# Kernel tuning notes

Measured on AMD Instinct MI355X. Metric: run time of the kernel, lower is better.

## Reference

```python
import jax, jax.numpy as jnp
import numpy as np

B, S1, S2, D1, D2 = 4, 2048, 2048, 512, 512
H, DK, DV = 8, 64, 64


def setup_inputs() -> dict:
    key = jax.random.key(0)
    ks = jax.random.split(key, 8)
    x1 = jax.random.normal(ks[0], (B, S1, D1), dtype=jnp.float32)
    x2 = jax.random.normal(ks[1], (B, S2, D2), dtype=jnp.float32)
    x3 = jax.random.normal(ks[2], (B, S2, D2), dtype=jnp.float32)
    s = 0.02
    Wq = jax.random.normal(ks[3], (D1, H * DK), dtype=jnp.float32) * s
    Wk = jax.random.normal(ks[4], (D2, H * DK), dtype=jnp.float32) * s
    Wv = jax.random.normal(ks[5], (D2, H * DV), dtype=jnp.float32) * s
    Wo = jax.random.normal(ks[6], (H * DV, D1), dtype=jnp.float32) * s
    bo = jnp.zeros((D1,), dtype=jnp.float32)
    return {"x1": x1, "x2": x2, "x3": x3, "Wq": Wq, "Wk": Wk, "Wv": Wv, "Wo": Wo, "bo": bo}


def reference(x1, x2, x3, Wq, Wk, Wv, Wo, bo):
    b, s1, _ = x1.shape
    # project to per-head q, k, v: [B, H, S, Dh]
    q = (x1 @ Wq).reshape(b, s1, H, DK).transpose(0, 2, 1, 3)
    k = (x2 @ Wk).reshape(b, x2.shape[1], H, DK).transpose(0, 2, 1, 3)
    v = (x3 @ Wv).reshape(b, x3.shape[1], H, DV).transpose(0, 2, 1, 3)
    scores = jnp.einsum('bhqd,bhkd->bhqk', q, k) / jnp.sqrt(jnp.float32(DK))
    attn = jax.nn.softmax(scores, axis=-1)
    out = jnp.einsum('bhqk,bhkd->bhqd', attn, v)  # [B, H, S1, DV]
    out = out.transpose(0, 2, 1, 3).reshape(b, s1, H * DV)
    return out @ Wo + bo
```

## Files before the change

kernel.cpp:

```cpp
#include <hip/hip_runtime.h>

typedef __attribute__((ext_vector_type(4))) float f32x4;
typedef __attribute__((ext_vector_type(16))) float f32x16;
typedef __attribute__((ext_vector_type(8))) __bf16 bf16x8;
typedef __attribute__((ext_vector_type(4))) __bf16 bf16x4;
typedef __attribute__((ext_vector_type(2))) __bf16 bf16x2;
typedef __attribute__((ext_vector_type(4))) unsigned u32x4;

#define DEVINL __device__ __forceinline__

DEVINL void gld16(const void* g, void* l) {
  __builtin_amdgcn_global_load_lds((__attribute__((address_space(1))) void*)(void*)g,
                                   (__attribute__((address_space(3))) void*)l, 16, 0, 0);
}


__global__ __launch_bounds__(256) void cvt_w(const float* Wq, const float* Wk, const float* Wv,
                                             const float* Wo, __bf16* WT) {
  __shared__ float t[64][65];
  const int l = blockIdx.x;
  const int z = l >> 6;
  const float* W = z == 0 ? Wq : z == 1 ? Wk : z == 2 ? Wv : Wo;
  __bf16* D = WT + (size_t)z * 512 * 512;
  const int r0 = ((l >> 3) & 7) * 64, c0 = (l & 7) * 64;
  const int tx = threadIdx.x & 63, ty = threadIdx.x >> 6;
#pragma unroll
  for (int j = 0; j < 16; ++j)
    t[ty + j * 4][tx] = W[(size_t)(r0 + ty + j * 4) * 512 + c0 + tx];
  __syncthreads();
#pragma unroll
  for (int j = 0; j < 16; ++j)
    D[(size_t)(c0 + ty + j * 4) * 512 + r0 + tx] = (__bf16)t[tx][ty + j * 4];
}


DEVINL void gemm_tile_f32(const float* A, const __bf16* Bt, int m0, int n0,
                          __bf16* As, __bf16* Bs, f32x4 acc[4][4]) {
  const int tid = threadIdx.x, lane = tid & 63, w = tid >> 6;
  const int qd = lane >> 4, r = lane & 15;
  const int wm = w & 1, wn = w >> 1;
  const char* bp[4];
#pragma unroll
  for (int j = 0; j < 4; ++j) {
    int c = (w * 4 + j) * 64 + lane;
    int row = c >> 3, gc = (c & 7) ^ (row & 7);
    bp[j] = (const char*)Bt + (size_t)(n0 + row) * 1024 + gc * 16;
  }
  const int am = tid >> 4, ac = tid & 15;
  const float* ap = A + (size_t)(m0 + am) * 512 + ac * 4;
  int woff[8];
#pragma unroll
  for (int j = 0; j < 8; ++j) {
    int m = j * 16 + am;
    woff[j] = m * 128 + (((ac >> 1) ^ (m & 7)) << 4) + ((ac & 1) << 3);
  }
  int offA[4][2], offB[4][2];
#pragma unroll
  for (int t = 0; t < 4; ++t)
#pragma unroll
    for (int ks = 0; ks < 2; ++ks) {
      int m = wm * 64 + t * 16 + r;
      offA[t][ks] = m * 128 + (((ks * 4 + qd) ^ (m & 7)) * 16);
      int n = wn * 64 + t * 16 + r;
      offB[t][ks] = n * 128 + (((ks * 4 + qd) ^ (n & 7)) * 16);
    }
  char* AsC = (char*)As;
  char* BsC = (char*)Bs;
  f32x4 areg[8];
  auto loadA = [&](int kt) {
#pragma unroll
    for (int j = 0; j < 8; ++j)
      areg[j] = *(const f32x4*)(ap + (size_t)j * 16 * 512 + kt * 64);
  };
  loadA(0);
  for (int kt = 0; kt < 8; ++kt) {
    __syncthreads();
#pragma unroll
    for (int j = 0; j < 4; ++j) gld16(bp[j] + kt * 128, BsC + (w * 4 + j) * 1024);
#pragma unroll
    for (int j = 0; j < 8; ++j) {
      bf16x4 o;
#pragma unroll
      for (int g = 0; g < 4; ++g) o[g] = (__bf16)areg[j][g];
      *(bf16x4*)(AsC + woff[j]) = o;
    }
    if (kt < 7) loadA(kt + 1);
    __syncthreads();
#pragma unroll
    for (int ks = 0; ks < 2; ++ks) {
      bf16x8 a[4], b[4];
#pragma unroll
      for (int t = 0; t < 4; ++t) {
        a[t] = *(const bf16x8*)(AsC + offA[t][ks]);
        b[t] = *(const bf16x8*)(BsC + offB[t][ks]);
      }
#pragma unroll
      for (int i = 0; i < 4; ++i)
#pragma unroll
        for (int j2 = 0; j2 < 4; ++j2)
          acc[i][j2] = __builtin_amdgcn_mfma_f32_16x16x32_bf16(a[i], b[j2], acc[i][j2], 0, 0, 0);
    }
  }
}

__global__ __launch_bounds__(256, 3) void gemm_proj(const float* x1, const float* x2,
                                                    const float* x3, const __bf16* WT,
                                                    __bf16* Qo, __bf16* Ko, __bf16* Vto) {
  __shared__ __align__(16) char smem[34816];
  __bf16* As = (__bf16*)smem;
  __bf16* Bs = (__bf16*)(smem + 16384);
  const int z = blockIdx.z;
  const float* A = z == 0 ? x1 : z == 1 ? x2 : x3;
  const __bf16* Bt = WT + (size_t)z * 512 * 512;
  const int l = blockIdx.x;
  const int sidx = l >> 3;
  const int m0 = ((l & 7) * 8 + (sidx >> 2)) * 128;
  const int n0 = (sidx & 3) * 128;
  f32x4 acc[4][4] = {};
  gemm_tile_f32(A, Bt, m0, n0, As, Bs, acc);
  const int tid = threadIdx.x, lane = tid & 63, w = tid >> 6;
  const int qd = lane >> 4, r = lane & 15, wm = w & 1, wn = w >> 1;
  const int b = m0 >> 11, sbase = m0 & 2047;
  if (z == 2) {
    __syncthreads();
    char* T = smem;
#pragma unroll
    for (int mt = 0; mt < 4; ++mt)
#pragma unroll
      for (int nt = 0; nt < 4; ++nt) {
        int dv = wn * 64 + nt * 16 + r;
        int sl = wm * 64 + mt * 16 + qd * 4;
        bf16x4 p4;
#pragma unroll
        for (int g = 0; g < 4; ++g) p4[g] = (__bf16)acc[mt][nt][g];
        *(bf16x4*)(T + (size_t)dv * 272 + sl * 2) = p4;
      }
    __syncthreads();
#pragma unroll
    for (int p2 = 0; p2 < 2; ++p2) {
      int dvrow = p2 * 64 + (tid >> 2);
      int col = n0 + dvrow, h = col >> 6, d = col & 63;
      __bf16* dst = Vto + ((size_t)(b * 8 + h) * 64 + d) * 2048 + sbase + (tid & 3) * 8;
#pragma unroll
      for (int j = 0; j < 4; ++j) {
        bf16x8 vv = *(const bf16x8*)(T + (size_t)dvrow * 272 + (tid & 3) * 16 + j * 64);
        *(bf16x8*)(dst + j * 32) = vv;
      }
    }
  } else {
    const float qscale = 0.18033688f;
#pragma unroll
    for (int mt = 0; mt < 4; ++mt) {
#pragma unroll
      for (int nt = 0; nt < 4; ++nt) {
        f32x4 v = acc[mt][nt];
        if (z == 0) {
#pragma unroll
          for (int g = 0; g < 4; ++g) v[g] *= qscale;
        }
        int col = n0 + wn * 64 + nt * 16 + r;
        int h = col >> 6, d = col & 63;
        int s = sbase + wm * 64 + mt * 16 + qd * 4;
        __bf16* O = (z == 0 ? Qo : Ko) + ((size_t)(b * 8 + h) * 2048 + s) * 64 + d;
#pragma unroll
        for (int g = 0; g < 4; ++g) O[(size_t)g * 64] = (__bf16)v[g];
      }
    }
  }
}

__global__ __launch_bounds__(256, 2) void gemm_out(const __bf16* Op, const float* Lp,
                                                   const __bf16* WoT, const float* bo,
                                                   float* out) {
  __shared__ __align__(16) __bf16 As[64 * 64];
  __shared__ __align__(16) __bf16 Bs[128 * 64];
  const int tid = threadIdx.x, lane = tid & 63, w = tid >> 6;
  const int qd = lane >> 4, r = lane & 15, wm = w & 1, wn = w >> 1;
  const int id = blockIdx.x;
  const int rest = id >> 3;
  const int m0 = ((id & 7) * 16 + (rest & 15)) * 64;
  const int n0 = (rest >> 4) * 128;
  const int b8 = (m0 >> 11) * 8;
  const int sb = m0 & 2047;
  const char* bp[4];
#pragma unroll
  for (int j = 0; j < 4; ++j) {
    int c = (w * 4 + j) * 64 + lane;
    int row = c >> 3, gc = (c & 7) ^ (row & 7);
    bp[j] = (const char*)WoT + (size_t)(n0 + row) * 1024 + gc * 16;
  }
  int arow[2], ach[2];
#pragma unroll
  for (int j = 0; j < 2; ++j) {
    int c = (w * 2 + j) * 64 + lane;
    arow[j] = c >> 3;
    ach[j] = c & 7;
  }
  int offA[2][2], offB[4][2];
#pragma unroll
  for (int ks = 0; ks < 2; ++ks) {
#pragma unroll
    for (int t = 0; t < 2; ++t) {
      int m = wm * 32 + t * 16 + r;
      offA[t][ks] = m * 128 + (((ks * 4 + qd) ^ (m & 7)) * 16);
    }
#pragma unroll
    for (int t = 0; t < 4; ++t) {
      int n = wn * 64 + t * 16 + r;
      offB[t][ks] = n * 128 + (((ks * 4 + qd) ^ (n & 7)) * 16);
    }
  }
  char* AsC = (char*)As;
  char* BsC = (char*)Bs;
  bf16x8 pa0[2], pa1[2];
  float pinv[2];
  auto loadA = [&](int h) {
#pragma unroll
    for (int j = 0; j < 2; ++j) {
      size_t rr = (size_t)(b8 + h) * 2048 + sb + arow[j];
      const __bf16* p0 = Op + rr * 64 + ach[j] * 8;
      pa0[j] = *(const bf16x8*)p0;
      pa1[j] = *(const bf16x8*)(p0 + (size_t)32 * 2048 * 64);
      pinv[j] = 1.0f / (Lp[rr] + Lp[rr + 65536]);
    }
  };
  loadA(0);
  f32x4 acc[2][4] = {};
  for (int kt = 0; kt < 8; ++kt) {
    __syncthreads();
#pragma unroll
    for (int j = 0; j < 4; ++j) gld16(bp[j] + kt * 128, BsC + (w * 4 + j) * 1024);
#pragma unroll
    for (int j = 0; j < 2; ++j) {
      bf16x8 q;
#pragma unroll
      for (int k2 = 0; k2 < 8; ++k2)
        q[k2] = (__bf16)(((float)pa0[j][k2] + (float)pa1[j][k2]) * pinv[j]);
      *(bf16x8*)(AsC + arow[j] * 128 + (ach[j] ^ (arow[j] & 7)) * 16) = q;
    }
    __syncthreads();
    if (kt < 7) loadA(kt + 1);
#pragma unroll
    for (int ks = 0; ks < 2; ++ks) {
      bf16x8 a[2], b[4];
#pragma unroll
      for (int t = 0; t < 2; ++t) a[t] = *(const bf16x8*)(AsC + offA[t][ks]);
#pragma unroll
      for (int t = 0; t < 4; ++t) b[t] = *(const bf16x8*)(BsC + offB[t][ks]);
#pragma unroll
      for (int i = 0; i < 2; ++i)
#pragma unroll
        for (int j2 = 0; j2 < 4; ++j2)
          acc[i][j2] = __builtin_amdgcn_mfma_f32_16x16x32_bf16(a[i], b[j2], acc[i][j2], 0, 0, 0);
    }
  }
#pragma unroll
  for (int nt = 0; nt < 4; ++nt) {
    int col = n0 + wn * 64 + nt * 16 + r;
    float bv = bo[col];
#pragma unroll
    for (int mt = 0; mt < 2; ++mt) {
      int mg = m0 + wm * 32 + mt * 16 + qd * 4;
#pragma unroll
      for (int g = 0; g < 4; ++g) out[(size_t)(mg + g) * 512 + col] = acc[mt][nt][g] + bv;
    }
  }
}

__global__ __launch_bounds__(256, 4) void attn(const __bf16* Q, const __bf16* K,
                                               const __bf16* Vt, __bf16* Opart, float* Lp) {
  __shared__ __align__(16) __bf16 Qs[128 * 64];
  __shared__ __align__(16) __bf16 Ksd[2][64 * 64];
  __shared__ __align__(16) __bf16 Vs[64 * 64];
  const int tid = threadIdx.x, lane = tid & 63, w = tid >> 6;
  const int l31 = lane & 31, lh = lane >> 5;
  const int id = blockIdx.x;
  const int rest = id >> 3;
  const int bh = (id & 7) * 4 + (rest >> 5);
  const int kvh = (rest >> 4) & 1;
  const int q0 = (rest & 15) * 128;
  const char* QgC = (const char*)(Q + ((size_t)bh * 2048 + q0) * 64);
  const char* KgC = (const char*)(K + (size_t)bh * 2048 * 64);
  const char* VgC = (const char*)(Vt + (size_t)bh * 64 * 2048);
  char* QsC = (char*)Qs;
  char* VsC = (char*)Vs;
  char* Kc = (char*)Ksd;
  char* Kn = (char*)Ksd + 8192;

  int koff[2], voff[2], ldso[2];
#pragma unroll
  for (int j = 0; j < 2; ++j) {
    int c = (w * 2 + j) * 64 + lane;
    int m = c >> 3, gc = (c & 7) ^ (m & 7);
    int ms = (m & ~12) | ((m & 4) << 1) | ((m & 8) >> 1);
    koff[j] = ms * 128 + gc * 16;
    voff[j] = m * 4096 + gc * 16;
    ldso[j] = (w * 2 + j) * 1024;
  }

  const int kt0 = kvh * 16;
  const size_t kb = (size_t)kt0 * 8192;
  const size_t vb = (size_t)kt0 * 128;

#pragma unroll
  for (int j = 0; j < 4; ++j) {
    int c = (w * 4 + j) * 64 + lane;
    int m = c >> 3, gc = (c & 7) ^ (m & 7);
    gld16(QgC + m * 128 + gc * 16, QsC + (w * 4 + j) * 1024);
  }
  gld16(KgC + kb + koff[0], Kc + ldso[0]);
  gld16(KgC + kb + koff[1], Kc + ldso[1]);
  gld16(VgC + vb + voff[0], VsC + ldso[0]);
  gld16(VgC + vb + voff[1], VsC + ldso[1]);
  gld16(KgC + kb + 8192 + koff[0], Kn + ldso[0]);
  gld16(KgC + kb + 8192 + koff[1], Kn + ldso[1]);
  __builtin_amdgcn_sched_barrier(0);
  asm volatile("s_waitcnt vmcnt(2)" ::: "memory");
  __builtin_amdgcn_sched_barrier(0);
  __builtin_amdgcn_s_barrier();
  __builtin_amdgcn_sched_barrier(0);

  const int rb = l31 * 128;
  const int he = (((lane & 7) ^ lh) << 4);
  const int qrow = (w * 32 + l31) * 128;

  bf16x8 ones;
#pragma unroll
  for (int j = 0; j < 8; ++j) ones[j] = (__bf16)1.0f;

  f32x16 oacc[2] = {};
  f32x16 lacc = {};
  bf16x8 pa[4];

  auto smhalf = [&](const f32x16& s, bf16x8& pa0, bf16x8& pa1) {
    unsigned wds[8];
#pragma unroll
    for (int i = 0; i < 8; ++i) {
      bf16x2 t;
      t[0] = (__bf16)__builtin_exp2f(s[2 * i]);
      t[1] = (__bf16)__builtin_exp2f(s[2 * i + 1]);
      wds[i] = __builtin_bit_cast(unsigned, t);
    }
    pa0 = __builtin_bit_cast(bf16x8, (u32x4){wds[0], wds[1], wds[2], wds[3]});
    pa1 = __builtin_bit_cast(bf16x8, (u32x4){wds[4], wds[5], wds[6], wds[7]});
  };
  auto qkchain = [&](const char* Kb, int half, const bf16x8 qf[4]) {
    f32x16 s = {};
#pragma unroll
    for (int c = 0; c < 4; ++c) {
      bf16x8 kf = *(const bf16x8*)(Kb + half * 4096 + rb + ((c << 5) ^ he));
      s = __builtin_amdgcn_mfma_f32_32x32x16_bf16(kf, qf[c], s, 0, 0, 0);
    }
    return s;
  };

  {
    bf16x8 qf[4];
#pragma unroll
    for (int c = 0; c < 4; ++c) qf[c] = *(const bf16x8*)(QsC + qrow + ((c << 5) ^ he));
    f32x16 s0 = qkchain(Kc, 0, qf);
    f32x16 s1 = qkchain(Kc, 1, qf);
    smhalf(s0, pa[0], pa[1]);
    smhalf(s1, pa[2], pa[3]);
  }
  __builtin_amdgcn_sched_barrier(0);
  asm volatile("s_waitcnt vmcnt(0)" ::: "memory");
  __builtin_amdgcn_sched_barrier(0);
  __builtin_amdgcn_s_barrier();
  __builtin_amdgcn_sched_barrier(0);

#pragma unroll 1
  for (int t = 0; t < 15; ++t) {
    __builtin_amdgcn_s_setprio(1);
#pragma unroll
    for (int c = 0; c < 4; ++c) {
      lacc = __builtin_amdgcn_mfma_f32_32x32x16_bf16(pa[c], ones, lacc, 0, 0, 0);
      bf16x8 vf0 = *(const bf16x8*)(VsC + rb + ((c << 5) ^ he));
      oacc[0] = __builtin_amdgcn_mfma_f32_32x32x16_bf16(pa[c], vf0, oacc[0], 0, 0, 0);
      bf16x8 vf1 = *(const bf16x8*)(VsC + 4096 + rb + ((c << 5) ^ he));
      oacc[1] = __builtin_amdgcn_mfma_f32_32x32x16_bf16(pa[c], vf1, oacc[1], 0, 0, 0);
    }
    bf16x8 qf[4];
#pragma unroll
    for (int c = 0; c < 4; ++c) qf[c] = *(const bf16x8*)(QsC + qrow + ((c << 5) ^ he));
    f32x16 s0 = qkchain(Kn, 0, qf);
    f32x16 s1 = qkchain(Kn, 1, qf);
    smhalf(s0, pa[0], pa[1]);
    __builtin_amdgcn_s_setprio(0);
    __builtin_amdgcn_sched_barrier(0);
    __builtin_amdgcn_s_barrier();
    __builtin_amdgcn_sched_barrier(0);

    gld16(VgC + vb + (size_t)(t + 1) * 128 + voff[0], VsC + ldso[0]);
    gld16(VgC + vb + (size_t)(t + 1) * 128 + voff[1], VsC + ldso[1]);
    if (t < 14) {
      gld16(KgC + kb + (size_t)(t + 2) * 8192 + koff[0], Kc + ldso[0]);
      gld16(KgC + kb + (size_t)(t + 2) * 8192 + koff[1], Kc + ldso[1]);
    }
    __builtin_amdgcn_sched_barrier(0);
    smhalf(s1, pa[2], pa[3]);
    __builtin_amdgcn_sched_barrier(0);
    asm volatile("s_waitcnt vmcnt(0)" ::: "memory");
    __builtin_amdgcn_sched_barrier(0);
    __builtin_amdgcn_s_barrier();
    __builtin_amdgcn_sched_barrier(0);

    char* tmp = Kc;
    Kc = Kn;
    Kn = tmp;
  }

#pragma unroll
  for (int c = 0; c < 4; ++c) {
    lacc = __builtin_amdgcn_mfma_f32_32x32x16_bf16(pa[c], ones, lacc, 0, 0, 0);
    bf16x8 vf0 = *(const bf16x8*)(VsC + rb + ((c << 5) ^ he));
    oacc[0] = __builtin_amdgcn_mfma_f32_32x32x16_bf16(pa[c], vf0, oacc[0], 0, 0, 0);
    bf16x8 vf1 = *(const bf16x8*)(VsC + 4096 + rb + ((c << 5) ^ he));
    oacc[1] = __builtin_amdgcn_mfma_f32_32x32x16_bf16(pa[c], vf1, oacc[1], 0, 0, 0);
  }

  const size_t pbase = (size_t)(kvh * 32 + bh) * 2048;
  if (l31 == 0) {
#pragma unroll
    for (int g = 0; g < 16; ++g)
      Lp[pbase + q0 + w * 32 + (g & 3) + 8 * (g >> 2) + 4 * lh] = lacc[g];
  }
  __bf16* Ob0 = Opart + pbase * 64;
#pragma unroll
  for (int dvt = 0; dvt < 2; ++dvt) {
#pragma unroll
    for (int g = 0; g < 16; ++g) {
      int s = q0 + w * 32 + (g & 3) + 8 * (g >> 2) + 4 * lh;
      Ob0[(size_t)s * 64 + dvt * 32 + l31] = (__bf16)oacc[dvt][g];
    }
  }
}


extern "C" void kernel_launch(void* const* d_in, const int* in_sizes, int n_in,
                              void* d_out, int out_size, void* d_ws, size_t ws_size,
                              hipStream_t stream) {
  const float* x1 = (const float*)d_in[0];
  const float* x2 = (const float*)d_in[1];
  const float* x3 = (const float*)d_in[2];
  const float* Wq = (const float*)d_in[3];
  const float* Wk = (const float*)d_in[4];
  const float* Wv = (const float*)d_in[5];
  const float* Wo = (const float*)d_in[6];
  const float* bo = (const float*)d_in[7];
  float* out = (float*)d_out;
  char* ws = (char*)d_ws;
  const size_t MB = 1ull << 20;
  __bf16* WT = (__bf16*)(ws + 24 * MB);
  __bf16* Qb = (__bf16*)(ws + 26 * MB);
  __bf16* Kb = (__bf16*)(ws + 34 * MB);
  __bf16* Vtb = (__bf16*)(ws + 42 * MB);
  __bf16* Opart = (__bf16*)(ws + 58 * MB);
  float* Lp = (float*)(ws + 74 * MB);

  cvt_w<<<dim3(256), 256, 0, stream>>>(Wq, Wk, Wv, Wo, WT);
  gemm_proj<<<dim3(256, 1, 3), 256, 0, stream>>>(x1, x2, x3, WT, Qb, Kb, Vtb);
  attn<<<dim3(1024), 256, 0, stream>>>(Qb, Kb, Vtb, Opart, Lp);
  gemm_out<<<dim3(512), 256, 0, stream>>>(Opart, Lp, WT + 3ull * 512 * 512, bo, out);
}
```

Before: 183.7 us.

## Widen projection GEMM tile to 128x256 to halve A conversion work

```diff
diff --git a/kernel.cpp b/kernel.cpp
--- a/kernel.cpp
+++ b/kernel.cpp
@@ -35,14 +35,14 @@
 
 
 DEVINL void gemm_tile_f32(const float* A, const __bf16* Bt, int m0, int n0,
-                          __bf16* As, __bf16* Bs, f32x4 acc[4][4]) {
+                          __bf16* As, __bf16* Bs, f32x4 acc[4][8]) {
   const int tid = threadIdx.x, lane = tid & 63, w = tid >> 6;
   const int qd = lane >> 4, r = lane & 15;
   const int wm = w & 1, wn = w >> 1;
-  const char* bp[4];
-#pragma unroll
-  for (int j = 0; j < 4; ++j) {
-    int c = (w * 4 + j) * 64 + lane;
+  const char* bp[8];
+#pragma unroll
+  for (int j = 0; j < 8; ++j) {
+    int c = (w * 8 + j) * 64 + lane;
     int row = c >> 3, gc = (c & 7) ^ (row & 7);
     bp[j] = (const char*)Bt + (size_t)(n0 + row) * 1024 + gc * 16;
   }
@@ -54,14 +54,19 @@
     int m = j * 16 + am;
     woff[j] = m * 128 + (((ac >> 1) ^ (m & 7)) << 4) + ((ac & 1) << 3);
   }
-  int offA[4][2], offB[4][2];
+  int offA[4][2], offB[8][2];
 #pragma unroll
   for (int t = 0; t < 4; ++t)
 #pragma unroll
     for (int ks = 0; ks < 2; ++ks) {
       int m = wm * 64 + t * 16 + r;
       offA[t][ks] = m * 128 + (((ks * 4 + qd) ^ (m & 7)) * 16);
-      int n = wn * 64 + t * 16 + r;
+    }
+#pragma unroll
+  for (int t = 0; t < 8; ++t)
+#pragma unroll
+    for (int ks = 0; ks < 2; ++ks) {
+      int n = wn * 128 + t * 16 + r;
       offB[t][ks] = n * 128 + (((ks * 4 + qd) ^ (n & 7)) * 16);
     }
   char* AsC = (char*)As;
@@ -76,7 +81,7 @@
   for (int kt = 0; kt < 8; ++kt) {
     __syncthreads();
 #pragma unroll
-    for (int j = 0; j < 4; ++j) gld16(bp[j] + kt * 128, BsC + (w * 4 + j) * 1024);
+    for (int j = 0; j < 8; ++j) gld16(bp[j] + kt * 128, BsC + (w * 8 + j) * 1024);
 #pragma unroll
     for (int j = 0; j < 8; ++j) {
       bf16x4 o;
@@ -88,63 +93,66 @@
     __syncthreads();
 #pragma unroll
     for (int ks = 0; ks < 2; ++ks) {
-      bf16x8 a[4], b[4];
-#pragma unroll
-      for (int t = 0; t < 4; ++t) {
-        a[t] = *(const bf16x8*)(AsC + offA[t][ks]);
-        b[t] = *(const bf16x8*)(BsC + offB[t][ks]);
+      bf16x8 a[4];
+#pragma unroll
+      for (int t = 0; t < 4; ++t) a[t] = *(const bf16x8*)(AsC + offA[t][ks]);
+#pragma unroll
+      for (int j2 = 0; j2 < 8; ++j2) {
+        bf16x8 b = *(const bf16x8*)(BsC + offB[j2][ks]);
+#pragma unroll
+        for (int i = 0; i < 4; ++i)
+          acc[i][j2] = __builtin_amdgcn_mfma_f32_16x16x32_bf16(a[i], b, acc[i][j2], 0, 0, 0);
       }
-#pragma unroll
-      for (int i = 0; i < 4; ++i)
-#pragma unroll
-        for (int j2 = 0; j2 < 4; ++j2)
-          acc[i][j2] = __builtin_amdgcn_mfma_f32_16x16x32_bf16(a[i], b[j2], acc[i][j2], 0, 0, 0);
-    }
-  }
-}
-
-__global__ __launch_bounds__(256, 3) void gemm_proj(const float* x1, const float* x2,
+    }
+  }
+}
+
+__global__ __launch_bounds__(256, 2) void gemm_proj(const float* x1, const float* x2,
                                                     const float* x3, const __bf16* WT,
                                                     __bf16* Qo, __bf16* Ko, __bf16* Vto) {
-  __shared__ __align__(16) char smem[34816];
+  __shared__ __align__(16) char smem[49152];
   __bf16* As = (__bf16*)smem;
   __bf16* Bs = (__bf16*)(smem + 16384);
   const int z = blockIdx.z;
   const float* A = z == 0 ? x1 : z == 1 ? x2 : x3;
   const __bf16* Bt = WT + (size_t)z * 512 * 512;
   const int l = blockIdx.x;
-  const int sidx = l >> 3;
-  const int m0 = ((l & 7) * 8 + (sidx >> 2)) * 128;
-  const int n0 = (sidx & 3) * 128;
-  f32x4 acc[4][4] = {};
+  const int m0 = ((l & 7) * 8 + (l >> 4)) * 128;
+  const int n0 = ((l >> 3) & 1) * 256;
+  f32x4 acc[4][8] = {};
   gemm_tile_f32(A, Bt, m0, n0, As, Bs, acc);
   const int tid = threadIdx.x, lane = tid & 63, w = tid >> 6;
   const int qd = lane >> 4, r = lane & 15, wm = w & 1, wn = w >> 1;
   const int b = m0 >> 11, sbase = m0 & 2047;
   if (z == 2) {
-    __syncthreads();
     char* T = smem;
 #pragma unroll
-    for (int mt = 0; mt < 4; ++mt)
-#pragma unroll
-      for (int nt = 0; nt < 4; ++nt) {
-        int dv = wn * 64 + nt * 16 + r;
-        int sl = wm * 64 + mt * 16 + qd * 4;
-        bf16x4 p4;
-#pragma unroll
-        for (int g = 0; g < 4; ++g) p4[g] = (__bf16)acc[mt][nt][g];
-        *(bf16x4*)(T + (size_t)dv * 272 + sl * 2) = p4;
+    for (int p = 0; p < 2; ++p) {
+      __syncthreads();
+      if (wn == p) {
+#pragma unroll
+        for (int mt = 0; mt < 4; ++mt)
+#pragma unroll
+          for (int nt = 0; nt < 8; ++nt) {
+            int dv = nt * 16 + r;
+            int sl = wm * 64 + mt * 16 + qd * 4;
+            bf16x4 p4;
+#pragma unroll
+            for (int g = 0; g < 4; ++g) p4[g] = (__bf16)acc[mt][nt][g];
+            *(bf16x4*)(T + (size_t)dv * 272 + sl * 2) = p4;
+          }
       }
-    __syncthreads();
-#pragma unroll
-    for (int p2 = 0; p2 < 2; ++p2) {
-      int dvrow = p2 * 64 + (tid >> 2);
-      int col = n0 + dvrow, h = col >> 6, d = col & 63;
-      __bf16* dst = Vto + ((size_t)(b * 8 + h) * 64 + d) * 2048 + sbase + (tid & 3) * 8;
-#pragma unroll
-      for (int j = 0; j < 4; ++j) {
-        bf16x8 vv = *(const bf16x8*)(T + (size_t)dvrow * 272 + (tid & 3) * 16 + j * 64);
-        *(bf16x8*)(dst + j * 32) = vv;
+      __syncthreads();
+#pragma unroll
+      for (int p2 = 0; p2 < 2; ++p2) {
+        int dvrow = p2 * 64 + (tid >> 2);
+        int col = n0 + p * 128 + dvrow, h = col >> 6, d = col & 63;
+        __bf16* dst = Vto + ((size_t)(b * 8 + h) * 64 + d) * 2048 + sbase + (tid & 3) * 8;
+#pragma unroll
+        for (int j = 0; j < 4; ++j) {
+          bf16x8 vv = *(const bf16x8*)(T + (size_t)dvrow * 272 + (tid & 3) * 16 + j * 64);
+          *(bf16x8*)(dst + j * 32) = vv;
+        }
       }
     }
   } else {
@@ -152,13 +160,13 @@
 #pragma unroll
     for (int mt = 0; mt < 4; ++mt) {
 #pragma unroll
-      for (int nt = 0; nt < 4; ++nt) {
+      for (int nt = 0; nt < 8; ++nt) {
         f32x4 v = acc[mt][nt];
         if (z == 0) {
 #pragma unroll
           for (int g = 0; g < 4; ++g) v[g] *= qscale;
         }
-        int col = n0 + wn * 64 + nt * 16 + r;
+        int col = n0 + wn * 128 + nt * 16 + r;
         int h = col >> 6, d = col & 63;
         int s = sbase + wm * 64 + mt * 16 + qd * 4;
         __bf16* O = (z == 0 ? Qo : Ko) + ((size_t)(b * 8 + h) * 2048 + s) * 64 + d;
@@ -459,7 +467,7 @@
   float* Lp = (float*)(ws + 74 * MB);
 
   cvt_w<<<dim3(256), 256, 0, stream>>>(Wq, Wk, Wv, Wo, WT);
-  gemm_proj<<<dim3(256, 1, 3), 256, 0, stream>>>(x1, x2, x3, WT, Qb, Kb, Vtb);
+  gemm_proj<<<dim3(128, 1, 3), 256, 0, stream>>>(x1, x2, x3, WT, Qb, Kb, Vtb);
   attn<<<dim3(1024), 256, 0, stream>>>(Qb, Kb, Vtb, Opart, Lp);
   gemm_out<<<dim3(512), 256, 0, stream>>>(Opart, Lp, WT + 3ull * 512 * 512, bo, out);
 }
```

New measurement: 185.5 us. About the same (+0.9%).

## Drop split-KV attention; normalize in-kernel and write output in GEMM layout

Applied to the files above, without the earlier changes.

```diff
diff --git a/kernel.cpp b/kernel.cpp
--- a/kernel.cpp
+++ b/kernel.cpp
@@ -169,9 +169,8 @@
   }
 }
 
-__global__ __launch_bounds__(256, 2) void gemm_out(const __bf16* Op, const float* Lp,
-                                                   const __bf16* WoT, const float* bo,
-                                                   float* out) {
+__global__ __launch_bounds__(256, 2) void gemm_out(const __bf16* Ob, const __bf16* WoT,
+                                                   const float* bo, float* out) {
   __shared__ __align__(16) __bf16 As[64 * 64];
   __shared__ __align__(16) __bf16 Bs[128 * 64];
   const int tid = threadIdx.x, lane = tid & 63, w = tid >> 6;
@@ -180,22 +179,20 @@
   const int rest = id >> 3;
   const int m0 = ((id & 7) * 16 + (rest & 15)) * 64;
   const int n0 = (rest >> 4) * 128;
-  const int b8 = (m0 >> 11) * 8;
-  const int sb = m0 & 2047;
+  const char* ap[2];
   const char* bp[4];
+#pragma unroll
+  for (int j = 0; j < 2; ++j) {
+    int c = (w * 2 + j) * 64 + lane;
+    int row = c >> 3, gc = (c & 7) ^ (row & 7);
+    ap[j] = (const char*)Ob + (size_t)(m0 + row) * 1024 + gc * 16;
+  }
 #pragma unroll
   for (int j = 0; j < 4; ++j) {
     int c = (w * 4 + j) * 64 + lane;
     int row = c >> 3, gc = (c & 7) ^ (row & 7);
     bp[j] = (const char*)WoT + (size_t)(n0 + row) * 1024 + gc * 16;
   }
-  int arow[2], ach[2];
-#pragma unroll
-  for (int j = 0; j < 2; ++j) {
-    int c = (w * 2 + j) * 64 + lane;
-    arow[j] = c >> 3;
-    ach[j] = c & 7;
-  }
   int offA[2][2], offB[4][2];
 #pragma unroll
   for (int ks = 0; ks < 2; ++ks) {
@@ -212,34 +209,14 @@
   }
   char* AsC = (char*)As;
   char* BsC = (char*)Bs;
-  bf16x8 pa0[2], pa1[2];
-  float pinv[2];
-  auto loadA = [&](int h) {
-#pragma unroll
-    for (int j = 0; j < 2; ++j) {
-      size_t rr = (size_t)(b8 + h) * 2048 + sb + arow[j];
-      const __bf16* p0 = Op + rr * 64 + ach[j] * 8;
-      pa0[j] = *(const bf16x8*)p0;
-      pa1[j] = *(const bf16x8*)(p0 + (size_t)32 * 2048 * 64);
-      pinv[j] = 1.0f / (Lp[rr] + Lp[rr + 65536]);
-    }
-  };
-  loadA(0);
   f32x4 acc[2][4] = {};
   for (int kt = 0; kt < 8; ++kt) {
     __syncthreads();
 #pragma unroll
+    for (int j = 0; j < 2; ++j) gld16(ap[j] + kt * 128, AsC + (w * 2 + j) * 1024);
+#pragma unroll
     for (int j = 0; j < 4; ++j) gld16(bp[j] + kt * 128, BsC + (w * 4 + j) * 1024);
-#pragma unroll
-    for (int j = 0; j < 2; ++j) {
-      bf16x8 q;
-#pragma unroll
-      for (int k2 = 0; k2 < 8; ++k2)
-        q[k2] = (__bf16)(((float)pa0[j][k2] + (float)pa1[j][k2]) * pinv[j]);
-      *(bf16x8*)(AsC + arow[j] * 128 + (ach[j] ^ (arow[j] & 7)) * 16) = q;
-    }
-    __syncthreads();
-    if (kt < 7) loadA(kt + 1);
+    __syncthreads();
 #pragma unroll
     for (int ks = 0; ks < 2; ++ks) {
       bf16x8 a[2], b[4];
@@ -268,7 +245,7 @@
 }
 
 __global__ __launch_bounds__(256, 4) void attn(const __bf16* Q, const __bf16* K,
-                                               const __bf16* Vt, __bf16* Opart, float* Lp) {
+                                               const __bf16* Vt, __bf16* Ob) {
   __shared__ __align__(16) __bf16 Qs[128 * 64];
   __shared__ __align__(16) __bf16 Ksd[2][64 * 64];
   __shared__ __align__(16) __bf16 Vs[64 * 64];
@@ -276,8 +253,7 @@
   const int l31 = lane & 31, lh = lane >> 5;
   const int id = blockIdx.x;
   const int rest = id >> 3;
-  const int bh = (id & 7) * 4 + (rest >> 5);
-  const int kvh = (rest >> 4) & 1;
+  const int bh = (id & 7) * 4 + (rest >> 4);
   const int q0 = (rest & 15) * 128;
   const char* QgC = (const char*)(Q + ((size_t)bh * 2048 + q0) * 64);
   const char* KgC = (const char*)(K + (size_t)bh * 2048 * 64);
@@ -298,22 +274,18 @@
     ldso[j] = (w * 2 + j) * 1024;
   }
 
-  const int kt0 = kvh * 16;
-  const size_t kb = (size_t)kt0 * 8192;
-  const size_t vb = (size_t)kt0 * 128;
-
 #pragma unroll
   for (int j = 0; j < 4; ++j) {
     int c = (w * 4 + j) * 64 + lane;
     int m = c >> 3, gc = (c & 7) ^ (m & 7);
     gld16(QgC + m * 128 + gc * 16, QsC + (w * 4 + j) * 1024);
   }
-  gld16(KgC + kb + koff[0], Kc + ldso[0]);
-  gld16(KgC + kb + koff[1], Kc + ldso[1]);
-  gld16(VgC + vb + voff[0], VsC + ldso[0]);
-  gld16(VgC + vb + voff[1], VsC + ldso[1]);
-  gld16(KgC + kb + 8192 + koff[0], Kn + ldso[0]);
-  gld16(KgC + kb + 8192 + koff[1], Kn + ldso[1]);
+  gld16(KgC + koff[0], Kc + ldso[0]);
+  gld16(KgC + koff[1], Kc + ldso[1]);
+  gld16(VgC + voff[0], VsC + ldso[0]);
+  gld16(VgC + voff[1], VsC + ldso[1]);
+  gld16(KgC + 8192 + koff[0], Kn + ldso[0]);
+  gld16(KgC + 8192 + koff[1], Kn + ldso[1]);
   __builtin_amdgcn_sched_barrier(0);
   asm volatile("s_waitcnt vmcnt(2)" ::: "memory");
   __builtin_amdgcn_sched_barrier(0);
@@ -370,7 +342,7 @@
   __builtin_amdgcn_sched_barrier(0);
 
 #pragma unroll 1
-  for (int t = 0; t < 15; ++t) {
+  for (int t = 0; t < 31; ++t) {
     __builtin_amdgcn_s_setprio(1);
 #pragma unroll
     for (int c = 0; c < 4; ++c) {
@@ -391,11 +363,11 @@
     __builtin_amdgcn_s_barrier();
     __builtin_amdgcn_sched_barrier(0);
 
-    gld16(VgC + vb + (size_t)(t + 1) * 128 + voff[0], VsC + ldso[0]);
-    gld16(VgC + vb + (size_t)(t + 1) * 128 + voff[1], VsC + ldso[1]);
-    if (t < 14) {
-      gld16(KgC + kb + (size_t)(t + 2) * 8192 + koff[0], Kc + ldso[0]);
-      gld16(KgC + kb + (size_t)(t + 2) * 8192 + koff[1], Kc + ldso[1]);
+    gld16(VgC + (size_t)(t + 1) * 128 + voff[0], VsC + ldso[0]);
+    gld16(VgC + (size_t)(t + 1) * 128 + voff[1], VsC + ldso[1]);
+    if (t < 30) {
+      gld16(KgC + (size_t)(t + 2) * 8192 + koff[0], Kc + ldso[0]);
+      gld16(KgC + (size_t)(t + 2) * 8192 + koff[1], Kc + ldso[1]);
     }
     __builtin_amdgcn_sched_barrier(0);
     smhalf(s1, pa[2], pa[3]);
@@ -419,20 +391,14 @@
     oacc[1] = __builtin_amdgcn_mfma_f32_32x32x16_bf16(pa[c], vf1, oacc[1], 0, 0, 0);
   }
 
-  const size_t pbase = (size_t)(kvh * 32 + bh) * 2048;
-  if (l31 == 0) {
-#pragma unroll
-    for (int g = 0; g < 16; ++g)
-      Lp[pbase + q0 + w * 32 + (g & 3) + 8 * (g >> 2) + 4 * lh] = lacc[g];
-  }
-  __bf16* Ob0 = Opart + pbase * 64;
-#pragma unroll
-  for (int dvt = 0; dvt < 2; ++dvt) {
-#pragma unroll
-    for (int g = 0; g < 16; ++g) {
-      int s = q0 + w * 32 + (g & 3) + 8 * (g >> 2) + 4 * lh;
-      Ob0[(size_t)s * 64 + dvt * 32 + l31] = (__bf16)oacc[dvt][g];
-    }
+  const int b = bh >> 3, h = bh & 7;
+  __bf16* ObG = Ob + ((size_t)(b * 2048 + q0)) * 512 + h * 64;
+#pragma unroll
+  for (int g = 0; g < 16; ++g) {
+    int ql = w * 32 + (g & 3) + 8 * (g >> 2) + 4 * lh;
+    float inv = 1.0f / lacc[g];
+    ObG[(size_t)ql * 512 + l31] = (__bf16)(oacc[0][g] * inv);
+    ObG[(size_t)ql * 512 + 32 + l31] = (__bf16)(oacc[1][g] * inv);
   }
 }
 
@@ -455,11 +421,10 @@
   __bf16* Qb = (__bf16*)(ws + 26 * MB);
   __bf16* Kb = (__bf16*)(ws + 34 * MB);
   __bf16* Vtb = (__bf16*)(ws + 42 * MB);
-  __bf16* Opart = (__bf16*)(ws + 58 * MB);
-  float* Lp = (float*)(ws + 74 * MB);
+  __bf16* Ob = (__bf16*)(ws + 50 * MB);
 
   cvt_w<<<dim3(256), 256, 0, stream>>>(Wq, Wk, Wv, Wo, WT);
   gemm_proj<<<dim3(256, 1, 3), 256, 0, stream>>>(x1, x2, x3, WT, Qb, Kb, Vtb);
-  attn<<<dim3(1024), 256, 0, stream>>>(Qb, Kb, Vtb, Opart, Lp);
-  gemm_out<<<dim3(512), 256, 0, stream>>>(Opart, Lp, WT + 3ull * 512 * 512, bo, out);
-}
+  attn<<<dim3(512), 256, 0, stream>>>(Qb, Kb, Vtb, Ob);
+  gemm_out<<<dim3(512), 256, 0, stream>>>(Ob, WT + 3ull * 512 * 512, bo, out);
+}
```

New measurement: 185.6 us. No clear change (+1.0%).
